# Optimization experiments

Measured on AMD Instinct MI355X. Metric: run time of the kernel, lower is better.

## Reference

```python
import jax, jax.numpy as jnp
import numpy as np

NUM_HEADS = 16
NUM_GROUPS = 2
HEAD_DIM = 128  # in_features // num_heads = 2048 // 16
MAX_POS = 512 + 256 + 256  # MAX_SEQ_LEN + SHARED_SLOTS + OUTPUT_SLOTS


def _rope_tables():
    inv_freq = 1.0 / 10000 ** (jnp.arange(0, HEAD_DIM, 2) / HEAD_DIM)
    t = jnp.arange(MAX_POS)
    freqs = jnp.outer(t, inv_freq)
    freqs = jnp.concatenate([freqs, freqs], axis=-1)  # [MAX_POS, HEAD_DIM]
    return jnp.sin(freqs), jnp.cos(freqs)


def _rotate_half(x):
    h = x.shape[-1] // 2
    x1, x2 = x[..., :h], x[..., h:]
    return jnp.concatenate([-x2, x1], axis=-1)


def setup_inputs() -> dict:
    key = jax.random.key(0)
    ks = jax.random.split(key, 5)
    b, s, d = 4, 1024, 2048
    kvd = NUM_GROUPS * HEAD_DIM
    sc = 1.0 / np.sqrt(d).astype(np.float32)
    return {
        "x": jax.random.normal(ks[0], (b, s, d), jnp.float32),
        "Wq": jax.random.normal(ks[1], (d, d), jnp.float32) * sc,
        "bq": jnp.zeros((d,), jnp.float32),
        "Wk": jax.random.normal(ks[2], (d, kvd), jnp.float32) * sc,
        "bk": jnp.zeros((kvd,), jnp.float32),
        "Wv": jax.random.normal(ks[3], (d, kvd), jnp.float32) * sc,
        "bv": jnp.zeros((kvd,), jnp.float32),
        "Wo": jax.random.normal(ks[4], (d, d), jnp.float32) * sc,
        "bo": jnp.zeros((d,), jnp.float32),
    }


def reference(x, Wq, bq, Wk, bk, Wv, bv, Wo, bo):
    b, s, d = x.shape
    sin, cos = _rope_tables()
    # original: sin_cached[q_pos, None, :] broadcasts over (b, s, heads, head_dim)
    sin = sin[:s][None, :, None, :]
    cos = cos[:s][None, :, None, :]

    q = (x @ Wq + bq).reshape(b, s, NUM_HEADS, HEAD_DIM)
    k = (x @ Wk + bk).reshape(b, s, NUM_GROUPS, HEAD_DIM)
    v = (x @ Wv + bv).reshape(b, s, NUM_GROUPS, HEAD_DIM)

    q = q * cos + _rotate_half(q) * sin
    k = k * cos + _rotate_half(k) * sin

    # GQA: avoid materializing expanded K/V by grouping the head dim of q.
    r = NUM_HEADS // NUM_GROUPS  # repeats per group
    qg = q.reshape(b, s, NUM_GROUPS, r, HEAD_DIM)
    scale = HEAD_DIM ** -0.5
    scores = jnp.einsum('bsgrd,btgd->bgrst', qg, k) * scale
    attn = jax.nn.softmax(scores, axis=-1)
    out = jnp.einsum('bgrst,btgd->bsgrd', attn, v).reshape(b, s, d)
    return out @ Wo + bo
```

## Files before the change

kernel.cpp:

```cpp
#include <hip/hip_runtime.h>
#include <hip/hip_bf16.h>
#include <hip/hip_fp16.h>
#include <math.h>

#define BATCH   4
#define SEQ     1024
#define DMODEL  2048
#define NHEADS  16
#define NGROUPS 2
#define HDIM    128
#define ROWS    (BATCH * SEQ)
#define NQKV    2560

typedef float    f32x4 __attribute__((ext_vector_type(4)));
typedef _Float16 f16x8 __attribute__((ext_vector_type(8)));

__device__ __forceinline__ void glds16(const void* g, void* s) {
    __builtin_amdgcn_global_load_lds(
        (__attribute__((address_space(1))) void*)g,
        (__attribute__((address_space(3))) void*)s, 16, 0, 0);
}

__device__ __forceinline__ float red16_max(float v) {
    v = fmaxf(v, __int_as_float(__builtin_amdgcn_mov_dpp(__float_as_int(v), 0xB1, 0xF, 0xF, true)));
    v = fmaxf(v, __int_as_float(__builtin_amdgcn_mov_dpp(__float_as_int(v), 0x4E, 0xF, 0xF, true)));
    v = fmaxf(v, __int_as_float(__builtin_amdgcn_mov_dpp(__float_as_int(v), 0x124, 0xF, 0xF, true)));
    v = fmaxf(v, __int_as_float(__builtin_amdgcn_mov_dpp(__float_as_int(v), 0x128, 0xF, 0xF, true)));
    return v;
}
__device__ __forceinline__ float red16_sum(float v) {
    v += __int_as_float(__builtin_amdgcn_mov_dpp(__float_as_int(v), 0xB1, 0xF, 0xF, true));
    v += __int_as_float(__builtin_amdgcn_mov_dpp(__float_as_int(v), 0x4E, 0xF, 0xF, true));
    v += __int_as_float(__builtin_amdgcn_mov_dpp(__float_as_int(v), 0x124, 0xF, 0xF, true));
    v += __int_as_float(__builtin_amdgcn_mov_dpp(__float_as_int(v), 0x128, 0xF, 0xF, true));
    return v;
}

__global__ void prep_const_kernel(float* __restrict__ sin_t, float* __restrict__ cos_t,
                                  const float* __restrict__ bq, const float* __restrict__ bk,
                                  const float* __restrict__ bv, float* __restrict__ bc) {
    int bid = blockIdx.x;
    if (bid < 256) {
        int idx = bid * 256 + threadIdx.x;
        int p = idx >> 6, j = idx & 63;
        float inv = powf(10000.0f, -(float)j * (1.0f / 64.0f));
        float f = (float)p * inv;
        sin_t[idx] = sinf(f);
        cos_t[idx] = cosf(f);
    } else {
        int i = (bid - 256) * 256 + threadIdx.x;
        if (i < NQKV)
            bc[i] = (i < 2048) ? bq[i] : ((i < 2304) ? bk[i - 2048] : bv[i - 2304]);
    }
}

__global__ void convert_x_kernel(const float* __restrict__ x, _Float16* __restrict__ xo) {
    int i = (blockIdx.x * 256 + threadIdx.x) * 8;
    float v[8];
    *reinterpret_cast<float4*>(&v[0]) = *reinterpret_cast<const float4*>(x + i);
    *reinterpret_cast<float4*>(&v[4]) = *reinterpret_cast<const float4*>(x + i + 4);
    f16x8 h;
#pragma unroll
    for (int j = 0; j < 8; ++j) h[j] = (_Float16)v[j];
    *reinterpret_cast<f16x8*>(xo + i) = h;
}

__global__ __launch_bounds__(256)
void transpose_w_all_kernel(const float* __restrict__ Wq, const float* __restrict__ Wk,
                            const float* __restrict__ Wv, const float* __restrict__ Wo,
                            _Float16* __restrict__ wqkv, _Float16* __restrict__ wot) {
    __shared__ float tile[64][65];
    int bx = blockIdx.x;
    const float* W; int ldw, drow0, nb; _Float16* dst;
    if (bx < 32)      { W = Wq; ldw = DMODEL; dst = wqkv; drow0 = 0;    nb = bx; }
    else if (bx < 36) { W = Wk; ldw = 256;    dst = wqkv; drow0 = 2048; nb = bx - 32; }
    else if (bx < 40) { W = Wv; ldw = 256;    dst = wqkv; drow0 = 2304; nb = bx - 36; }
    else              { W = Wo; ldw = DMODEL; dst = wot;  drow0 = 0;    nb = bx - 40; }
    int n0 = nb * 64, k0 = blockIdx.y * 64;
#pragma unroll
    for (int it = 0; it < 16; ++it) {
        int e = it * 256 + threadIdx.x;
        int r = e >> 6, c = e & 63;
        tile[r][c] = W[(size_t)(k0 + r) * ldw + n0 + c];
    }
    __syncthreads();
#pragma unroll
    for (int it = 0; it < 16; ++it) {
        int e = it * 256 + threadIdx.x;
        int nr = e >> 6, kc = e & 63;
        dst[(size_t)(drow0 + n0 + nr) * DMODEL + k0 + kc] = (_Float16)tile[kc][nr];
    }
}

template<int OUT_HALF>
__global__ __launch_bounds__(256, 3)
void gemm_fp16_kernel(const _Float16* __restrict__ A, const _Float16* __restrict__ Bt,
                      const float* __restrict__ bias, void* __restrict__ Cout,
                      int M, int N, int K) {
    __shared__ __align__(16) _Float16 lds[16384];
    _Float16* As = lds;
    _Float16* Bs = lds + 8192;

    const int tid  = threadIdx.x;
    const int lane = tid & 63;
    const int w    = tid >> 6;
    const int nbn  = N >> 7;
    const int nwg  = gridDim.x;
    const int cpx  = nwg >> 3;
    const int bid  = blockIdx.x;
    const int swz  = (bid & 7) * cpx + (bid >> 3);
    const int row0 = (swz / nbn) << 7;
    const int col0 = (swz % nbn) << 7;
    const int wr   = (w >> 1) << 6;
    const int wc   = (w & 1) << 6;

    const f32x4 fz = {0.f, 0.f, 0.f, 0.f};
    f32x4 acc[4][4];
#pragma unroll
    for (int i = 0; i < 4; ++i)
#pragma unroll
        for (int j = 0; j < 4; ++j) acc[i][j] = fz;

    for (int k0 = 0; k0 < K; k0 += 64) {
        __syncthreads();
#pragma unroll
        for (int it = 0; it < 4; ++it) {
            int chunk = it * 256 + tid;
            int trow  = chunk >> 3;
            int jp    = chunk & 7;
            int j     = jp ^ (trow & 7);
            size_t aoff = (size_t)(row0 + trow) * K + k0 + j * 8;
            size_t boff = (size_t)(col0 + trow) * K + k0 + j * 8;
            int ldst = (it * 256 + (tid & 192)) * 16;
            glds16(A  + aoff, (char*)As + ldst);
            glds16(Bt + boff, (char*)Bs + ldst);
        }
        __syncthreads();

#pragma unroll
        for (int ks = 0; ks < 2; ++ks) {
            f16x8 a4[4], b4[4];
            int ja = ks * 4 + (lane >> 4);
#pragma unroll
            for (int i = 0; i < 4; ++i) {
                int ar = wr + i * 16 + (lane & 15);
                a4[i] = *reinterpret_cast<const f16x8*>(
                    (const char*)As + ar * 128 + ((ja ^ (ar & 7)) << 4));
                int br = wc + i * 16 + (lane & 15);
                b4[i] = *reinterpret_cast<const f16x8*>(
                    (const char*)Bs + br * 128 + ((ja ^ (br & 7)) << 4));
            }
#pragma unroll
            for (int i = 0; i < 4; ++i)
#pragma unroll
                for (int j = 0; j < 4; ++j)
                    acc[i][j] = __builtin_amdgcn_mfma_f32_16x16x32_f16(a4[i], b4[j], acc[i][j], 0, 0, 0);
        }
    }

    float bv4[4];
#pragma unroll
    for (int j = 0; j < 4; ++j) bv4[j] = bias[col0 + wc + j * 16 + (lane & 15)];
#pragma unroll
    for (int i = 0; i < 4; ++i)
#pragma unroll
        for (int j = 0; j < 4; ++j)
#pragma unroll
            for (int r = 0; r < 4; ++r) {
                int grow = row0 + wr + i * 16 + ((lane >> 4) << 2) + r;
                int gcol = col0 + wc + j * 16 + (lane & 15);
                float v = acc[i][j][r] + bv4[j];
                if (OUT_HALF)
                    ((_Float16*)Cout)[(size_t)grow * N + gcol] = (_Float16)v;
                else
                    ((float*)Cout)[(size_t)grow * N + gcol] = v;
            }
}

__global__ __launch_bounds__(256)
void prep_kv_kernel(const _Float16* __restrict__ qkv,
                    const float* __restrict__ sin_t, const float* __restrict__ cos_t,
                    _Float16* __restrict__ kh, _Float16* __restrict__ vt) {
    __shared__ _Float16 tile[64][72];
    int s0 = blockIdx.x * 64, bg = blockIdx.y;
    int b = bg >> 1, g = bg & 1;

#pragma unroll
    for (int it = 0; it < 2; ++it) {
        int u = it * 256 + threadIdx.x;
        int r = u >> 3, jc = u & 7;
        int s = s0 + r;
        int j0 = jc * 8;
        const _Float16* src = qkv + (size_t)(b * SEQ + s) * NQKV + 2048 + g * HDIM;
        _Float16* dst = kh + ((size_t)bg * SEQ + s) * HDIM;
        f16x8 x1 = *reinterpret_cast<const f16x8*>(src + j0);
        f16x8 x2 = *reinterpret_cast<const f16x8*>(src + j0 + 64);
        float cc[8], ss[8];
        *reinterpret_cast<float4*>(&cc[0]) = *reinterpret_cast<const float4*>(cos_t + s * 64 + j0);
        *reinterpret_cast<float4*>(&cc[4]) = *reinterpret_cast<const float4*>(cos_t + s * 64 + j0 + 4);
        *reinterpret_cast<float4*>(&ss[0]) = *reinterpret_cast<const float4*>(sin_t + s * 64 + j0);
        *reinterpret_cast<float4*>(&ss[4]) = *reinterpret_cast<const float4*>(sin_t + s * 64 + j0 + 4);
        f16x8 o1, o2;
#pragma unroll
        for (int j = 0; j < 8; ++j) {
            float f1 = (float)x1[j], f2 = (float)x2[j];
            o1[j] = (_Float16)(f1 * cc[j] - f2 * ss[j]);
            o2[j] = (_Float16)(f2 * cc[j] + f1 * ss[j]);
        }
        *reinterpret_cast<f16x8*>(dst + j0)      = o1;
        *reinterpret_cast<f16x8*>(dst + j0 + 64) = o2;
    }

#pragma unroll
    for (int half = 0; half < 2; ++half) {
        int d0 = half * 64;
        __syncthreads();
#pragma unroll
        for (int it = 0; it < 2; ++it) {
            int c = it * 256 + threadIdx.x;
            int r = c >> 3, cc = (c & 7) * 8;
            f16x8 v = *reinterpret_cast<const f16x8*>(
                qkv + (size_t)(b * SEQ + s0 + r) * NQKV + 2304 + g * HDIM + d0 + cc);
#pragma unroll
            for (int j = 0; j < 8; ++j) tile[r][cc + j] = v[j];
        }
        __syncthreads();
#pragma unroll
        for (int it = 0; it < 2; ++it) {
            int c = it * 256 + threadIdx.x;
            int dr = c >> 3, sc = (c & 7) * 8;
            f16x8 o;
#pragma unroll
            for (int j = 0; j < 8; ++j) o[j] = tile[sc + j][dr];
            *reinterpret_cast<f16x8*>(vt + ((size_t)bg * HDIM + d0 + dr) * SEQ + s0 + sc) = o;
        }
    }
}

__global__ __launch_bounds__(256, 2)
void attn_kernel(const _Float16* __restrict__ qkv, const _Float16* __restrict__ kh,
                 const _Float16* __restrict__ vt,
                 const float* __restrict__ sin_t, const float* __restrict__ cos_t,
                 _Float16* __restrict__ ao) {
    __shared__ __align__(16) char smem[81920];

    const int tid = threadIdx.x, lane = tid & 63, w = tid >> 6;
    const int qt0 = blockIdx.x << 7;
    const int h = blockIdx.y, b = blockIdx.z;
    const int g = h >> 3;
    const _Float16* kbase = kh + (size_t)(b * NGROUPS + g) * SEQ * HDIM;
    const _Float16* vbase = vt + (size_t)(b * NGROUPS + g) * HDIM * SEQ;

    {
        char* Kb = smem;
        char* Vb = smem + 16384;
#pragma unroll
        for (int it = 0; it < 4; ++it) {
            int c = it * 256 + tid;
            int row = c >> 4, jc = c & 15;
            int sj = jc ^ (row & 7);
            glds16((const char*)(kbase + (size_t)row * HDIM) + (sj << 4),
                   Kb + (it * 256 + (tid & 192)) * 16);
        }
#pragma unroll
        for (int it = 0; it < 4; ++it) {
            int c = it * 256 + tid;
            int d = c >> 3, jc = c & 7;
            int sj = jc ^ (d & 7);
            glds16((const char*)(vbase + (size_t)d * SEQ) + (sj << 4),
                   Vb + (it * 256 + (tid & 192)) * 16);
        }
    }

    const int sl = lane >> 4;
    f16x8 af[2][4];
#pragma unroll
    for (int m = 0; m < 2; ++m) {
        int srow = qt0 + w * 32 + m * 16 + (lane & 15);
        const _Float16* qrp = qkv + (size_t)(b * SEQ + srow) * NQKV + h * HDIM;
#pragma unroll
        for (int ks = 0; ks < 4; ++ks)
            af[m][ks] = *reinterpret_cast<const f16x8*>(qrp + (ks * 4 + sl) * 8);
        const float qsc = 0.12751741f;
#pragma unroll
        for (int ks = 0; ks < 2; ++ks) {
            int d0 = (ks * 4 + sl) * 8;
            float cc[8], ss[8];
            *reinterpret_cast<float4*>(&cc[0]) = *reinterpret_cast<const float4*>(cos_t + srow * 64 + d0);
            *reinterpret_cast<float4*>(&cc[4]) = *reinterpret_cast<const float4*>(cos_t + srow * 64 + d0 + 4);
            *reinterpret_cast<float4*>(&ss[0]) = *reinterpret_cast<const float4*>(sin_t + srow * 64 + d0);
            *reinterpret_cast<float4*>(&ss[4]) = *reinterpret_cast<const float4*>(sin_t + srow * 64 + d0 + 4);
#pragma unroll
            for (int j = 0; j < 8; ++j) {
                float f1 = (float)af[m][ks][j], f2 = (float)af[m][ks + 2][j];
                af[m][ks][j]     = (_Float16)((f1 * cc[j] - f2 * ss[j]) * qsc);
                af[m][ks + 2][j] = (_Float16)((f2 * cc[j] + f1 * ss[j]) * qsc);
            }
        }
    }

    float m_run[2][4], l_run[2][4];
#pragma unroll
    for (int m = 0; m < 2; ++m)
#pragma unroll
        for (int r = 0; r < 4; ++r) { m_run[m][r] = -1e30f; l_run[m][r] = 0.f; }
    const f32x4 fz = {0.f, 0.f, 0.f, 0.f};
    f32x4 oacc[2][8];
#pragma unroll
    for (int m = 0; m < 2; ++m)
#pragma unroll
        for (int i = 0; i < 8; ++i) oacc[m][i] = fz;

    char* Pw = smem + 65536 + w * 4096;
    const int prow = lane & 15;

    int cur = 0;
    for (int t = 0; t < SEQ / 64; ++t) {
        char* Kb = smem + (cur << 15);
        char* Vb = Kb + 16384;
        if (t < SEQ / 64 - 1) {
            char* Kn = smem + ((cur ^ 1) << 15);
            char* Vn = Kn + 16384;
            int t0n = (t + 1) << 6;
#pragma unroll
            for (int it = 0; it < 4; ++it) {
                int c = it * 256 + tid;
                int row = c >> 4, jc = c & 15;
                int sj = jc ^ (row & 7);
                glds16((const char*)(kbase + (size_t)(t0n + row) * HDIM) + (sj << 4),
                       Kn + (it * 256 + (tid & 192)) * 16);
            }
#pragma unroll
            for (int it = 0; it < 4; ++it) {
                int c = it * 256 + tid;
                int d = c >> 3, jc = c & 7;
                int sj = jc ^ (d & 7);
                glds16((const char*)(vbase + (size_t)d * SEQ + t0n) + (sj << 4),
                       Vn + (it * 256 + (tid & 192)) * 16);
            }
            asm volatile("s_waitcnt vmcnt(8)" ::: "memory");
        } else {
            asm volatile("s_waitcnt vmcnt(0)" ::: "memory");
        }
        asm volatile("s_barrier" ::: "memory");

        f32x4 sacc[2][4];
#pragma unroll
        for (int m = 0; m < 2; ++m)
#pragma unroll
            for (int i = 0; i < 4; ++i) sacc[m][i] = fz;
#pragma unroll
        for (int ks = 0; ks < 4; ++ks) {
#pragma unroll
            for (int nf = 0; nf < 4; ++nf) {
                int trow = nf * 16 + (lane & 15);
                f16x8 bf = *reinterpret_cast<const f16x8*>(
                    Kb + trow * 256 + (((ks * 4 + (lane >> 4)) ^ (trow & 7)) << 4));
                sacc[0][nf] = __builtin_amdgcn_mfma_f32_16x16x32_f16(af[0][ks], bf, sacc[0][nf], 0, 0, 0);
                sacc[1][nf] = __builtin_amdgcn_mfma_f32_16x16x32_f16(af[1][ks], bf, sacc[1][nf], 0, 0, 0);
            }
        }

        float pm[2][4];
        float growth = -1e30f;
#pragma unroll
        for (int m = 0; m < 2; ++m)
#pragma unroll
            for (int r = 0; r < 4; ++r) {
                float v = fmaxf(fmaxf(sacc[m][0][r], sacc[m][1][r]),
                                fmaxf(sacc[m][2][r], sacc[m][3][r]));
                v = red16_max(v);
                pm[m][r] = v;
                growth = fmaxf(growth, v - m_run[m][r]);
            }
        if (__any(growth > 11.0f)) {
            float scl[2][4];
#pragma unroll
            for (int m = 0; m < 2; ++m)
#pragma unroll
                for (int r = 0; r < 4; ++r) {
                    float mn = fmaxf(m_run[m][r], pm[m][r]);
                    scl[m][r] = __builtin_amdgcn_exp2f(m_run[m][r] - mn);
                    m_run[m][r] = mn;
                    l_run[m][r] *= scl[m][r];
                }
#pragma unroll
            for (int m = 0; m < 2; ++m)
#pragma unroll
                for (int i = 0; i < 8; ++i) {
                    f32x4 o = oacc[m][i];
                    o[0] *= scl[m][0]; o[1] *= scl[m][1];
                    o[2] *= scl[m][2]; o[3] *= scl[m][3];
                    oacc[m][i] = o;
                }
        }
#pragma unroll
        for (int m = 0; m < 2; ++m)
#pragma unroll
            for (int r = 0; r < 4; ++r) {
                float ps = 0.f;
#pragma unroll
                for (int nf = 0; nf < 4; ++nf) {
                    float p = __builtin_amdgcn_exp2f(sacc[m][nf][r] - m_run[m][r]);
                    sacc[m][nf][r] = p;
                    ps += p;
                }
                l_run[m][r] += ps;
            }

#pragma unroll
        for (int m = 0; m < 2; ++m)
#pragma unroll
            for (int nf = 0; nf < 4; ++nf)
#pragma unroll
                for (int r = 0; r < 4; ++r) {
                    int pr = m * 16 + ((lane >> 4) << 2) + r;
                    int pc = nf * 16 + (lane & 15);
                    int byte = pr * 128 + ((pc * 2) ^ ((pr & 7) << 4));
                    *reinterpret_cast<_Float16*>(Pw + byte) = (_Float16)sacc[m][nf][r];
                }

#pragma unroll
        for (int ks = 0; ks < 2; ++ks) {
            int chP = ks * 4 + (lane >> 4);
            f16x8 pa[2];
#pragma unroll
            for (int m = 0; m < 2; ++m)
                pa[m] = *reinterpret_cast<const f16x8*>(
                    Pw + (m * 16 + prow) * 128 + ((chP ^ (prow & 7)) << 4));
#pragma unroll
            for (int nf = 0; nf < 8; ++nf) {
                int vrow = nf * 16 + (lane & 15);
                f16x8 vf = *reinterpret_cast<const f16x8*>(
                    Vb + vrow * 128 + (((ks * 4 + (lane >> 4)) ^ (vrow & 7)) << 4));
                oacc[0][nf] = __builtin_amdgcn_mfma_f32_16x16x32_f16(pa[0], vf, oacc[0][nf], 0, 0, 0);
                oacc[1][nf] = __builtin_amdgcn_mfma_f32_16x16x32_f16(pa[1], vf, oacc[1][nf], 0, 0, 0);
            }
        }

        asm volatile("s_barrier" ::: "memory");
        cur ^= 1;
    }

    float linv[2][4];
#pragma unroll
    for (int m = 0; m < 2; ++m)
#pragma unroll
        for (int r = 0; r < 4; ++r)
            linv[m][r] = 1.0f / red16_sum(l_run[m][r]);
#pragma unroll
    for (int m = 0; m < 2; ++m)
#pragma unroll
        for (int nf = 0; nf < 8; ++nf)
#pragma unroll
            for (int r = 0; r < 4; ++r) {
                int qr  = qt0 + w * 32 + m * 16 + ((lane >> 4) << 2) + r;
                int col = h * HDIM + nf * 16 + (lane & 15);
                float v = oacc[m][nf][r] * linv[m][r];
                ao[(size_t)(b * SEQ + qr) * DMODEL + col] = (_Float16)v;
            }
}

extern "C" void kernel_launch(void* const* d_in, const int* in_sizes, int n_in,
                              void* d_out, int out_size, void* d_ws, size_t ws_size,
                              hipStream_t stream) {
    const float* x  = (const float*)d_in[0];
    const float* Wq = (const float*)d_in[1];
    const float* bq = (const float*)d_in[2];
    const float* Wk = (const float*)d_in[3];
    const float* bk = (const float*)d_in[4];
    const float* Wv = (const float*)d_in[5];
    const float* bv = (const float*)d_in[6];
    const float* Wo = (const float*)d_in[7];
    const float* bo = (const float*)d_in[8];
    float* out = (float*)d_out;

    char* ws = (char*)d_ws;
    _Float16* xs     = (_Float16*)(ws);
    _Float16* wqkv16 = (_Float16*)(ws + 16777216);
    _Float16* wot16  = (_Float16*)(ws + 27262976);
    _Float16* qkv16  = (_Float16*)(ws + 35651584);
    _Float16* khb    = (_Float16*)(ws + 56623104);
    _Float16* vtb    = (_Float16*)(ws + 58720256);
    float*    sint   = (float*)(ws + 60817408);
    float*    cost   = (float*)(ws + 61079552);
    float*    bias_c = (float*)(ws + 61341696);
    _Float16* ao = xs;

    prep_const_kernel<<<266, 256, 0, stream>>>(sint, cost, bq, bk, bv, bias_c);
    convert_x_kernel<<<ROWS * DMODEL / 8 / 256, 256, 0, stream>>>(x, xs);
    transpose_w_all_kernel<<<dim3(72, 32), 256, 0, stream>>>(Wq, Wk, Wv, Wo, wqkv16, wot16);

    gemm_fp16_kernel<1><<<(ROWS / 128) * (NQKV / 128), 256, 0, stream>>>(
        xs, wqkv16, bias_c, qkv16, ROWS, NQKV, DMODEL);

    prep_kv_kernel<<<dim3(SEQ / 64, BATCH * NGROUPS), 256, 0, stream>>>(
        qkv16, sint, cost, khb, vtb);

    attn_kernel<<<dim3(SEQ / 128, NHEADS, BATCH), 256, 0, stream>>>(
        qkv16, khb, vtb, sint, cost, ao);

    gemm_fp16_kernel<0><<<(ROWS / 128) * (DMODEL / 128), 256, 0, stream>>>(
        ao, wot16, bo, out, ROWS, DMODEL, DMODEL);
}
```

Baseline: 267.0 us.

## Merge prep kernels into one launch and transpose QK^T MFMA for row-local softmax

Merges the three preprocessing kernels (x conversion, weight transpose, sin/cos/bias setup) into a single launch to cut launch overhead and inter-kernel gaps. In the attention kernel it swaps the MFMA operands for S = QK^T so each lane holds scores for one query row. The row max and sum then need only two cross-lane shuffles instead of per-register DPP reductions, and P is written to LDS as packed 4-element vectors instead of scalar halves. Rescale factors and the final normalizer are redistributed to the output layout with ds_bpermute, which adds some LDS-path traffic. The merged prep kernel reserves 64x65 floats of shared memory in every block, including the conversion blocks that never use it, which may lower occupancy for that part.

```diff
diff --git a/kernel.cpp b/kernel.cpp
--- a/kernel.cpp
+++ b/kernel.cpp
@@ -14,6 +14,7 @@
 
 typedef float    f32x4 __attribute__((ext_vector_type(4)));
 typedef _Float16 f16x8 __attribute__((ext_vector_type(8)));
+typedef _Float16 f16x4 __attribute__((ext_vector_type(4)));
 
 __device__ __forceinline__ void glds16(const void* g, void* s) {
     __builtin_amdgcn_global_load_lds(
@@ -21,74 +22,61 @@
         (__attribute__((address_space(3))) void*)s, 16, 0, 0);
 }
 
-__device__ __forceinline__ float red16_max(float v) {
-    v = fmaxf(v, __int_as_float(__builtin_amdgcn_mov_dpp(__float_as_int(v), 0xB1, 0xF, 0xF, true)));
-    v = fmaxf(v, __int_as_float(__builtin_amdgcn_mov_dpp(__float_as_int(v), 0x4E, 0xF, 0xF, true)));
-    v = fmaxf(v, __int_as_float(__builtin_amdgcn_mov_dpp(__float_as_int(v), 0x124, 0xF, 0xF, true)));
-    v = fmaxf(v, __int_as_float(__builtin_amdgcn_mov_dpp(__float_as_int(v), 0x128, 0xF, 0xF, true)));
-    return v;
-}
-__device__ __forceinline__ float red16_sum(float v) {
-    v += __int_as_float(__builtin_amdgcn_mov_dpp(__float_as_int(v), 0xB1, 0xF, 0xF, true));
-    v += __int_as_float(__builtin_amdgcn_mov_dpp(__float_as_int(v), 0x4E, 0xF, 0xF, true));
-    v += __int_as_float(__builtin_amdgcn_mov_dpp(__float_as_int(v), 0x124, 0xF, 0xF, true));
-    v += __int_as_float(__builtin_amdgcn_mov_dpp(__float_as_int(v), 0x128, 0xF, 0xF, true));
-    return v;
-}
-
-__global__ void prep_const_kernel(float* __restrict__ sin_t, float* __restrict__ cos_t,
-                                  const float* __restrict__ bq, const float* __restrict__ bk,
-                                  const float* __restrict__ bv, float* __restrict__ bc) {
+__global__ __launch_bounds__(256)
+void prep_all_kernel(const float* __restrict__ x, _Float16* __restrict__ xo,
+                     const float* __restrict__ Wq, const float* __restrict__ Wk,
+                     const float* __restrict__ Wv, const float* __restrict__ Wo,
+                     _Float16* __restrict__ wqkv, _Float16* __restrict__ wot,
+                     float* __restrict__ sin_t, float* __restrict__ cos_t,
+                     const float* __restrict__ bq, const float* __restrict__ bk,
+                     const float* __restrict__ bv, float* __restrict__ bc) {
+    __shared__ float tile[64][65];
     int bid = blockIdx.x;
-    if (bid < 256) {
-        int idx = bid * 256 + threadIdx.x;
-        int p = idx >> 6, j = idx & 63;
-        float inv = powf(10000.0f, -(float)j * (1.0f / 64.0f));
-        float f = (float)p * inv;
-        sin_t[idx] = sinf(f);
-        cos_t[idx] = cosf(f);
+    if (bid < 4096) {
+        int i = (bid * 256 + threadIdx.x) * 8;
+        float v[8];
+        *reinterpret_cast<float4*>(&v[0]) = *reinterpret_cast<const float4*>(x + i);
+        *reinterpret_cast<float4*>(&v[4]) = *reinterpret_cast<const float4*>(x + i + 4);
+        f16x8 h;
+#pragma unroll
+        for (int j = 0; j < 8; ++j) h[j] = (_Float16)v[j];
+        *reinterpret_cast<f16x8*>(xo + i) = h;
+    } else if (bid < 6400) {
+        int tb = bid - 4096;
+        int bx = tb % 72, by = tb / 72;
+        const float* W; int ldw, drow0, nb; _Float16* dst;
+        if (bx < 32)      { W = Wq; ldw = DMODEL; dst = wqkv; drow0 = 0;    nb = bx; }
+        else if (bx < 36) { W = Wk; ldw = 256;    dst = wqkv; drow0 = 2048; nb = bx - 32; }
+        else if (bx < 40) { W = Wv; ldw = 256;    dst = wqkv; drow0 = 2304; nb = bx - 36; }
+        else              { W = Wo; ldw = DMODEL; dst = wot;  drow0 = 0;    nb = bx - 40; }
+        int n0 = nb * 64, k0 = by * 64;
+#pragma unroll
+        for (int it = 0; it < 16; ++it) {
+            int e = it * 256 + threadIdx.x;
+            int r = e >> 6, c = e & 63;
+            tile[r][c] = W[(size_t)(k0 + r) * ldw + n0 + c];
+        }
+        __syncthreads();
+#pragma unroll
+        for (int it = 0; it < 16; ++it) {
+            int e = it * 256 + threadIdx.x;
+            int nr = e >> 6, kc = e & 63;
+            dst[(size_t)(drow0 + n0 + nr) * DMODEL + k0 + kc] = (_Float16)tile[kc][nr];
+        }
     } else {
-        int i = (bid - 256) * 256 + threadIdx.x;
-        if (i < NQKV)
-            bc[i] = (i < 2048) ? bq[i] : ((i < 2304) ? bk[i - 2048] : bv[i - 2304]);
-    }
-}
-
-__global__ void convert_x_kernel(const float* __restrict__ x, _Float16* __restrict__ xo) {
-    int i = (blockIdx.x * 256 + threadIdx.x) * 8;
-    float v[8];
-    *reinterpret_cast<float4*>(&v[0]) = *reinterpret_cast<const float4*>(x + i);
-    *reinterpret_cast<float4*>(&v[4]) = *reinterpret_cast<const float4*>(x + i + 4);
-    f16x8 h;
-#pragma unroll
-    for (int j = 0; j < 8; ++j) h[j] = (_Float16)v[j];
-    *reinterpret_cast<f16x8*>(xo + i) = h;
-}
-
-__global__ __launch_bounds__(256)
-void transpose_w_all_kernel(const float* __restrict__ Wq, const float* __restrict__ Wk,
-                            const float* __restrict__ Wv, const float* __restrict__ Wo,
-                            _Float16* __restrict__ wqkv, _Float16* __restrict__ wot) {
-    __shared__ float tile[64][65];
-    int bx = blockIdx.x;
-    const float* W; int ldw, drow0, nb; _Float16* dst;
-    if (bx < 32)      { W = Wq; ldw = DMODEL; dst = wqkv; drow0 = 0;    nb = bx; }
-    else if (bx < 36) { W = Wk; ldw = 256;    dst = wqkv; drow0 = 2048; nb = bx - 32; }
-    else if (bx < 40) { W = Wv; ldw = 256;    dst = wqkv; drow0 = 2304; nb = bx - 36; }
-    else              { W = Wo; ldw = DMODEL; dst = wot;  drow0 = 0;    nb = bx - 40; }
-    int n0 = nb * 64, k0 = blockIdx.y * 64;
-#pragma unroll
-    for (int it = 0; it < 16; ++it) {
-        int e = it * 256 + threadIdx.x;
-        int r = e >> 6, c = e & 63;
-        tile[r][c] = W[(size_t)(k0 + r) * ldw + n0 + c];
-    }
-    __syncthreads();
-#pragma unroll
-    for (int it = 0; it < 16; ++it) {
-        int e = it * 256 + threadIdx.x;
-        int nr = e >> 6, kc = e & 63;
-        dst[(size_t)(drow0 + n0 + nr) * DMODEL + k0 + kc] = (_Float16)tile[kc][nr];
+        int b2 = bid - 6400;
+        if (b2 < 256) {
+            int idx = b2 * 256 + threadIdx.x;
+            int p = idx >> 6, j = idx & 63;
+            float inv = powf(10000.0f, -(float)j * (1.0f / 64.0f));
+            float f = (float)p * inv;
+            sin_t[idx] = sinf(f);
+            cos_t[idx] = cosf(f);
+        } else {
+            int i = (b2 - 256) * 256 + threadIdx.x;
+            if (i < NQKV)
+                bc[i] = (i < 2048) ? bq[i] : ((i < 2304) ? bk[i - 2048] : bv[i - 2304]);
+        }
     }
 }
 
@@ -245,6 +233,8 @@
     __shared__ __align__(16) char smem[81920];
 
     const int tid = threadIdx.x, lane = tid & 63, w = tid >> 6;
+    const int qv  = lane & 15;
+    const int grp = lane >> 4;
     const int qt0 = blockIdx.x << 7;
     const int h = blockIdx.y, b = blockIdx.z;
     const int g = h >> 3;
@@ -272,19 +262,18 @@
         }
     }
 
-    const int sl = lane >> 4;
     f16x8 af[2][4];
 #pragma unroll
     for (int m = 0; m < 2; ++m) {
-        int srow = qt0 + w * 32 + m * 16 + (lane & 15);
+        int srow = qt0 + w * 32 + m * 16 + qv;
         const _Float16* qrp = qkv + (size_t)(b * SEQ + srow) * NQKV + h * HDIM;
 #pragma unroll
         for (int ks = 0; ks < 4; ++ks)
-            af[m][ks] = *reinterpret_cast<const f16x8*>(qrp + (ks * 4 + sl) * 8);
+            af[m][ks] = *reinterpret_cast<const f16x8*>(qrp + (ks * 4 + grp) * 8);
         const float qsc = 0.12751741f;
 #pragma unroll
         for (int ks = 0; ks < 2; ++ks) {
-            int d0 = (ks * 4 + sl) * 8;
+            int d0 = (ks * 4 + grp) * 8;
             float cc[8], ss[8];
             *reinterpret_cast<float4*>(&cc[0]) = *reinterpret_cast<const float4*>(cos_t + srow * 64 + d0);
             *reinterpret_cast<float4*>(&cc[4]) = *reinterpret_cast<const float4*>(cos_t + srow * 64 + d0 + 4);
@@ -299,11 +288,8 @@
         }
     }
 
-    float m_run[2][4], l_run[2][4];
-#pragma unroll
-    for (int m = 0; m < 2; ++m)
-#pragma unroll
-        for (int r = 0; r < 4; ++r) { m_run[m][r] = -1e30f; l_run[m][r] = 0.f; }
+    float m_run[2] = {-1e30f, -1e30f};
+    float l_run[2] = {0.f, 0.f};
     const f32x4 fz = {0.f, 0.f, 0.f, 0.f};
     f32x4 oacc[2][8];
 #pragma unroll
@@ -312,7 +298,6 @@
         for (int i = 0; i < 8; ++i) oacc[m][i] = fz;
 
     char* Pw = smem + 65536 + w * 4096;
-    const int prow = lane & 15;
 
     int cur = 0;
     for (int t = 0; t < SEQ / 64; ++t) {
@@ -353,86 +338,93 @@
         for (int ks = 0; ks < 4; ++ks) {
 #pragma unroll
             for (int nf = 0; nf < 4; ++nf) {
-                int trow = nf * 16 + (lane & 15);
-                f16x8 bf = *reinterpret_cast<const f16x8*>(
-                    Kb + trow * 256 + (((ks * 4 + (lane >> 4)) ^ (trow & 7)) << 4));
-                sacc[0][nf] = __builtin_amdgcn_mfma_f32_16x16x32_f16(af[0][ks], bf, sacc[0][nf], 0, 0, 0);
-                sacc[1][nf] = __builtin_amdgcn_mfma_f32_16x16x32_f16(af[1][ks], bf, sacc[1][nf], 0, 0, 0);
-            }
-        }
-
-        float pm[2][4];
-        float growth = -1e30f;
-#pragma unroll
-        for (int m = 0; m < 2; ++m)
-#pragma unroll
-            for (int r = 0; r < 4; ++r) {
-                float v = fmaxf(fmaxf(sacc[m][0][r], sacc[m][1][r]),
-                                fmaxf(sacc[m][2][r], sacc[m][3][r]));
-                v = red16_max(v);
-                pm[m][r] = v;
-                growth = fmaxf(growth, v - m_run[m][r]);
-            }
+                int trow = nf * 16 + qv;
+                f16x8 kf = *reinterpret_cast<const f16x8*>(
+                    Kb + trow * 256 + (((ks * 4 + grp) ^ (trow & 7)) << 4));
+                sacc[0][nf] = __builtin_amdgcn_mfma_f32_16x16x32_f16(kf, af[0][ks], sacc[0][nf], 0, 0, 0);
+                sacc[1][nf] = __builtin_amdgcn_mfma_f32_16x16x32_f16(kf, af[1][ks], sacc[1][nf], 0, 0, 0);
+            }
+        }
+
+        float pm2[2];
+#pragma unroll
+        for (int m = 0; m < 2; ++m) {
+            float v = sacc[m][0][0];
+#pragma unroll
+            for (int nf = 0; nf < 4; ++nf)
+#pragma unroll
+                for (int r = 0; r < 4; ++r) v = fmaxf(v, sacc[m][nf][r]);
+            v = fmaxf(v, __shfl_xor(v, 16));
+            v = fmaxf(v, __shfl_xor(v, 32));
+            pm2[m] = v;
+        }
+        float growth = fmaxf(pm2[0] - m_run[0], pm2[1] - m_run[1]);
         if (__any(growth > 11.0f)) {
-            float scl[2][4];
+            float scl[2];
+#pragma unroll
+            for (int m = 0; m < 2; ++m) {
+                float mn = fmaxf(m_run[m], pm2[m]);
+                scl[m] = __builtin_amdgcn_exp2f(m_run[m] - mn);
+                m_run[m] = mn;
+                l_run[m] *= scl[m];
+            }
+            float sclo[2][4];
 #pragma unroll
             for (int m = 0; m < 2; ++m)
 #pragma unroll
-                for (int r = 0; r < 4; ++r) {
-                    float mn = fmaxf(m_run[m][r], pm[m][r]);
-                    scl[m][r] = __builtin_amdgcn_exp2f(m_run[m][r] - mn);
-                    m_run[m][r] = mn;
-                    l_run[m][r] *= scl[m][r];
-                }
+                for (int r = 0; r < 4; ++r)
+                    sclo[m][r] = __int_as_float(__builtin_amdgcn_ds_bpermute(
+                        ((grp << 2) + r) << 2, __float_as_int(scl[m])));
 #pragma unroll
             for (int m = 0; m < 2; ++m)
 #pragma unroll
                 for (int i = 0; i < 8; ++i) {
                     f32x4 o = oacc[m][i];
-                    o[0] *= scl[m][0]; o[1] *= scl[m][1];
-                    o[2] *= scl[m][2]; o[3] *= scl[m][3];
+                    o[0] *= sclo[m][0]; o[1] *= sclo[m][1];
+                    o[2] *= sclo[m][2]; o[3] *= sclo[m][3];
                     oacc[m][i] = o;
                 }
         }
 #pragma unroll
-        for (int m = 0; m < 2; ++m)
-#pragma unroll
-            for (int r = 0; r < 4; ++r) {
-                float ps = 0.f;
-#pragma unroll
-                for (int nf = 0; nf < 4; ++nf) {
-                    float p = __builtin_amdgcn_exp2f(sacc[m][nf][r] - m_run[m][r]);
+        for (int m = 0; m < 2; ++m) {
+            float ps = 0.f;
+#pragma unroll
+            for (int nf = 0; nf < 4; ++nf)
+#pragma unroll
+                for (int r = 0; r < 4; ++r) {
+                    float p = __builtin_amdgcn_exp2f(sacc[m][nf][r] - m_run[m]);
                     sacc[m][nf][r] = p;
                     ps += p;
                 }
-                l_run[m][r] += ps;
-            }
+            l_run[m] += ps;
+        }
 
 #pragma unroll
         for (int m = 0; m < 2; ++m)
 #pragma unroll
-            for (int nf = 0; nf < 4; ++nf)
-#pragma unroll
-                for (int r = 0; r < 4; ++r) {
-                    int pr = m * 16 + ((lane >> 4) << 2) + r;
-                    int pc = nf * 16 + (lane & 15);
-                    int byte = pr * 128 + ((pc * 2) ^ ((pr & 7) << 4));
-                    *reinterpret_cast<_Float16*>(Pw + byte) = (_Float16)sacc[m][nf][r];
-                }
+            for (int nf = 0; nf < 4; ++nf) {
+                f16x4 pk;
+#pragma unroll
+                for (int r = 0; r < 4; ++r) pk[r] = (_Float16)sacc[m][nf][r];
+                int byte = m * 2048 + qv * 128 + nf * 32 + grp * 8;
+                byte ^= (qv & 7) << 4;
+                *reinterpret_cast<f16x4*>(Pw + byte) = pk;
+            }
 
 #pragma unroll
         for (int ks = 0; ks < 2; ++ks) {
-            int chP = ks * 4 + (lane >> 4);
             f16x8 pa[2];
 #pragma unroll
-            for (int m = 0; m < 2; ++m)
-                pa[m] = *reinterpret_cast<const f16x8*>(
-                    Pw + (m * 16 + prow) * 128 + ((chP ^ (prow & 7)) << 4));
+            for (int m = 0; m < 2; ++m) {
+                int byte = m * 2048 + qv * 128 + ks * 64 + grp * 16;
+                byte ^= (qv & 7) << 4;
+                pa[m] = *reinterpret_cast<const f16x8*>(Pw + byte);
+            }
 #pragma unroll
             for (int nf = 0; nf < 8; ++nf) {
-                int vrow = nf * 16 + (lane & 15);
+                int vrow = nf * 16 + qv;
                 f16x8 vf = *reinterpret_cast<const f16x8*>(
-                    Vb + vrow * 128 + (((ks * 4 + (lane >> 4)) ^ (vrow & 7)) << 4));
+                    Vb + vrow * 128 + (((ks * 4 + grp) ^ (vrow & 7)) << 4));
                 oacc[0][nf] = __builtin_amdgcn_mfma_f32_16x16x32_f16(pa[0], vf, oacc[0][nf], 0, 0, 0);
                 oacc[1][nf] = __builtin_amdgcn_mfma_f32_16x16x32_f16(pa[1], vf, oacc[1][nf], 0, 0, 0);
             }
@@ -442,21 +434,27 @@
         cur ^= 1;
     }
 
-    float linv[2][4];
+    float linvo[2][4];
+#pragma unroll
+    for (int m = 0; m < 2; ++m) {
+        float ls = l_run[m];
+        ls += __shfl_xor(ls, 16);
+        ls += __shfl_xor(ls, 32);
+        float linv = 1.0f / ls;
+#pragma unroll
+        for (int r = 0; r < 4; ++r)
+            linvo[m][r] = __int_as_float(__builtin_amdgcn_ds_bpermute(
+                ((grp << 2) + r) << 2, __float_as_int(linv)));
+    }
 #pragma unroll
     for (int m = 0; m < 2; ++m)
 #pragma unroll
-        for (int r = 0; r < 4; ++r)
-            linv[m][r] = 1.0f / red16_sum(l_run[m][r]);
-#pragma unroll
-    for (int m = 0; m < 2; ++m)
-#pragma unroll
         for (int nf = 0; nf < 8; ++nf)
 #pragma unroll
             for (int r = 0; r < 4; ++r) {
-                int qr  = qt0 + w * 32 + m * 16 + ((lane >> 4) << 2) + r;
-                int col = h * HDIM + nf * 16 + (lane & 15);
-                float v = oacc[m][nf][r] * linv[m][r];
+                int qr  = qt0 + w * 32 + m * 16 + (grp << 2) + r;
+                int col = h * HDIM + nf * 16 + qv;
+                float v = oacc[m][nf][r] * linvo[m][r];
                 ao[(size_t)(b * SEQ + qr) * DMODEL + col] = (_Float16)v;
             }
 }
@@ -487,9 +485,9 @@
     float*    bias_c = (float*)(ws + 61341696);
     _Float16* ao = xs;
 
-    prep_const_kernel<<<266, 256, 0, stream>>>(sint, cost, bq, bk, bv, bias_c);
-    convert_x_kernel<<<ROWS * DMODEL / 8 / 256, 256, 0, stream>>>(x, xs);
-    transpose_w_all_kernel<<<dim3(72, 32), 256, 0, stream>>>(Wq, Wk, Wv, Wo, wqkv16, wot16);
+    prep_all_kernel<<<6666, 256, 0, stream>>>(x, xs, Wq, Wk, Wv, Wo,
+                                              wqkv16, wot16, sint, cost,
+                                              bq, bk, bv, bias_c);
 
     gemm_fp16_kernel<1><<<(ROWS / 128) * (NQKV / 128), 256, 0, stream>>>(
         xs, wqkv16, bias_c, qkv16, ROWS, NQKV, DMODEL);
```

New measurement: 266.2 us. About the same (-0.3%).
